# Optimization experiments

Measured on AMD Instinct MI355X. Metric: run time of the kernel, lower is better.

## Reference

```python
import jax, jax.numpy as jnp
import numpy as np

B, T, HID = 4, 4096, 768
H, D = 12, 64
N_HASHES = 2
BUCKET_SIZE = T // 32          # reformer repo config: max_seq_len // 32 = 128
N_BUCKETS = T // BUCKET_SIZE   # 32
SELF_ATTN_VALUE = -5e4         # reformer_pytorch TOKEN_SELF_ATTN_VALUE
MASK_VALUE = -1e9


def lsh_attention(X, mask_bool, W_qk, W_v, rotations):
    # X: [b, t, hid]; rotations: [d, n_hashes, n_buckets//2] (shared across batch & heads)
    b, t, _ = X.shape
    d, n_hashes, half_nb = rotations.shape
    n_buckets = 2 * half_nb
    h = W_qk.shape[0] // d
    scale = d ** -0.5

    qk = X @ W_qk.T            # shared query/key projection (bias-free in reformer_pytorch)
    v = X @ W_v.T

    def merge_heads(x):  # [b,t,h*d] -> [b*h, t, d]
        return x.reshape(b, t, h, d).transpose(0, 2, 1, 3).reshape(b * h, t, d)

    qk, v = merge_heads(qk), merge_heads(v)
    maskbh = jnp.repeat(mask_bool, h, axis=0)          # [bh, t]

    # --- LSH bucketing ---
    rotated = jnp.einsum('btf,fhi->bhti', qk, rotations)          # [bh, nh, t, nb/2]
    rotated = jnp.concatenate([rotated, -rotated], axis=-1)       # [bh, nh, t, nb]
    buckets = jnp.argmax(rotated, axis=-1)                        # [bh, nh, t]
    offsets = (jnp.arange(n_hashes) * n_buckets)[None, :, None]
    buckets = (buckets + offsets).reshape(b * h, n_hashes * t)

    # --- stable sort by (bucket, position) ---
    total = n_hashes * t
    ticker = jnp.arange(total)[None, :]
    buckets_and_t = buckets * t + (ticker % t)
    sticker = jnp.argsort(buckets_and_t, axis=-1)   # stable
    undo = jnp.argsort(sticker, axis=-1)
    st = sticker % t                                 # original positions, sorted order

    sqk = jnp.take_along_axis(qk, st[..., None], axis=1)
    sv = jnp.take_along_axis(v, st[..., None], axis=1)
    smask = jnp.take_along_axis(maskbh, st, axis=1)

    # --- chunk; each chunk attends to itself + previous chunk ---
    n_chunks = n_hashes * n_buckets
    cl = total // n_chunks                                  # == bucket_size
    bq_t = st.reshape(b * h, n_chunks, cl)
    bqk = sqk.reshape(b * h, n_chunks, cl, d)
    bv = sv.reshape(b * h, n_chunks, cl, d)
    bmask = smask.reshape(b * h, n_chunks, cl)

    bq = bqk
    bk = bqk / jnp.clip(jnp.linalg.norm(bqk, axis=-1, keepdims=True), 1e-12)

    def look_one_back(x):
        return jnp.concatenate([x, jnp.roll(x, 1, axis=1)], axis=2)

    bk, bv = look_one_back(bk), look_one_back(bv)
    bkv_t = look_one_back(bq_t)
    bkv_mask = look_one_back(bmask)

    dots = jnp.einsum('bnie,bnje->bnij', bq, bk) * scale    # [bh, n_chunks, cl, 2cl]
    pad = bmask[..., :, None] & bkv_mask[..., None, :]
    dots = jnp.where(pad, dots, MASK_VALUE)
    self_mask = bq_t[..., :, None] == bkv_t[..., None, :]
    dots = jnp.where(self_mask, SELF_ATTN_VALUE, dots)

    lse = jax.scipy.special.logsumexp(dots, axis=-1, keepdims=True)
    probs = jnp.exp(dots - lse)
    bo = jnp.einsum('bnij,bnje->bnie', probs, bv)

    # --- unsort and combine hash rounds via softmax over round logsumexps ---
    so = bo.reshape(b * h, total, d)
    slogits = lse.reshape(b * h, total)
    o = jnp.take_along_axis(so, undo[..., None], axis=1)
    logits = jnp.take_along_axis(slogits, undo, axis=1)

    o = o.reshape(b * h, n_hashes, t, d)
    logits = logits.reshape(b * h, n_hashes, t, 1)
    round_probs = jnp.exp(logits - jax.scipy.special.logsumexp(logits, axis=1, keepdims=True))
    out = jnp.sum(o * round_probs, axis=1)                  # [bh, t, d]
    return out.reshape(b, h, t, d).transpose(0, 2, 1, 3).reshape(b, t, h * d)


def setup_inputs() -> dict:
    key = jax.random.key(0)
    ks = jax.random.split(key, 8)
    s = 1.0 / np.sqrt(HID)
    return {
        'X': jax.random.normal(ks[0], (B, T, HID), jnp.float32),
        'mask': jnp.ones((B, T), jnp.float32),
        'W_qk': jax.random.uniform(ks[1], (H * D, HID), jnp.float32, -s, s),
        'W_v': jax.random.uniform(ks[2], (H * D, HID), jnp.float32, -s, s),
        'rotations': jax.random.normal(ks[3], (D, N_HASHES, N_BUCKETS // 2), jnp.float32),
        'W_to': jax.random.uniform(ks[4], (HID, H * D), jnp.float32, -s, s),
        'b_to': jnp.zeros((HID,), jnp.float32),
        'W_o': jax.random.uniform(ks[5], (HID, HID), jnp.float32, -s, s),
        'b_o': jnp.zeros((HID,), jnp.float32),
    }


def reference(X, mask, W_qk, W_v, rotations, W_to, b_to, W_o, b_o):
    attn = lsh_attention(X, mask.astype(bool), W_qk, W_v, rotations)
    attn = attn @ W_to.T + b_to     # LSHSelfAttention.to_out
    return attn @ W_o.T + b_o       # ReformerAttention.W_o
```

## Files before the change

kernel.cpp:

```cpp
#include <hip/hip_runtime.h>
#include <hip/hip_bf16.h>
#include <math.h>


typedef __attribute__((ext_vector_type(8))) short bf16x8;
typedef __attribute__((ext_vector_type(4))) float f32x4;
typedef __attribute__((ext_vector_type(4))) double f64x4;

__device__ __forceinline__ float bf_lo(unsigned int w) { return __uint_as_float(w << 16); }
__device__ __forceinline__ float bf_hi(unsigned int w) { return __uint_as_float(w & 0xffff0000u); }
__device__ __forceinline__ float load_in(const void* p, size_t i, bool f32) {
  return f32 ? ((const float*)p)[i]
             : __bfloat162float(((const __hip_bfloat16*)p)[i]);
}
__device__ __forceinline__ unsigned short f2bf(float x) {
  __hip_bfloat16 h = __float2bfloat16(x);
  return *reinterpret_cast<unsigned short*>(&h);
}
__device__ __forceinline__ float bf2f(unsigned short u) { return __uint_as_float(((unsigned int)u) << 16); }

__global__ void k_detect(const unsigned int* __restrict__ X, int* __restrict__ flag) {
  if (threadIdx.x == 0 && blockIdx.x == 0) {
    int vote = 0;
    for (int i = 0; i < 64; ++i) {
      unsigned int e = (X[i] >> 7) & 0xffu;
      vote += (e >= 100u && e <= 141u) ? 1 : 0;
    }
    *flag = (vote < 32) ? 1 : 0;
  }
}

__global__ __launch_bounds__(256) void k_convert(
    const void* __restrict__ src, unsigned short* __restrict__ dst, int n8,
    const int* __restrict__ flag) {
  const bool f32in = (*flag != 0);
  int i = blockIdx.x * 256 + threadIdx.x;
  if (i >= n8) return;
  if (f32in) {
    const float4* s = (const float4*)src + (size_t)i * 2;
    float4 a = s[0], b = s[1];
    union { unsigned short u[8]; uint4 v; } o;
    o.u[0] = f2bf(a.x); o.u[1] = f2bf(a.y); o.u[2] = f2bf(a.z); o.u[3] = f2bf(a.w);
    o.u[4] = f2bf(b.x); o.u[5] = f2bf(b.y); o.u[6] = f2bf(b.z); o.u[7] = f2bf(b.w);
    ((uint4*)dst)[i] = o.v;
  } else {
    ((uint4*)dst)[i] = ((const uint4*)src)[i];
  }
}

__global__ __launch_bounds__(256) void k_build_wrot(
    const void* __restrict__ Wqk, const void* __restrict__ rot,
    double* __restrict__ WrotT, const int* __restrict__ flag) {
  const bool f32in = (*flag != 0);
  int idx = blockIdx.x * 256 + threadIdx.x;
  if (idx >= 768 * 384) return;
  int row = idx % 384;
  int c   = idx / 384;
  int hh = row >> 5, hi = row & 31;
  double s = 0.0;
  for (int f = 0; f < 64; ++f) {
    double rv = (double)load_in(rot, f * 32 + hi, f32in);
    double wv = (double)load_in(Wqk, (size_t)(hh * 64 + f) * 768 + c, f32in);
    s = fma(rv, wv, s);
  }
  WrotT[(size_t)c * 384 + row] = s;
}

__global__ __launch_bounds__(512) void k_bucket(
    const void* __restrict__ X, const double* __restrict__ WrotT,
    unsigned char* __restrict__ cls, const int* __restrict__ flag) {
  const bool f32in = (*flag != 0);
  __shared__ double SH[7296];
  double* Sc = SH;
  const int tid = threadIdx.x;
  const int M0 = blockIdx.x * 128;
  const int N0 = blockIdx.y * 96;
  const int w = tid >> 6, lane = tid & 63;
  const int l15 = lane & 15, lq = lane >> 4;
  const int sr = tid >> 2, sh2 = tid & 3;
  const int wk = tid >> 5, wn3 = (tid & 31) * 3;

  f64x4 acc[6];
  #pragma unroll
  for (int j = 0; j < 6; ++j) acc[j] = (f64x4){0.0, 0.0, 0.0, 0.0};

  int rowid[4], colid[4];
  {
    f64x4 zz = (f64x4){0.0, 0.0, 0.0, 0.0};
    f64x4 pr = __builtin_amdgcn_mfma_f64_16x16x4f64(
        (double)l15, (lq == 0) ? 1.0 : 0.0, zz, 0, 0, 0);
    f64x4 pc = __builtin_amdgcn_mfma_f64_16x16x4f64(
        (lq == 0) ? 1.0 : 0.0, (double)l15, zz, 0, 0, 0);
    #pragma unroll
    for (int r = 0; r < 4; ++r) {
      rowid[r] = (int)pr[r];
      colid[r] = (int)pc[r];
    }
  }

  double xv[4];
  double wvv[3];
  auto load_chunk = [&](int k0) {
    size_t base = (size_t)(M0 + sr) * 768 + k0 + sh2 * 4;
    if (f32in) {
      float4 f0 = *(const float4*)((const float*)X + base);
      xv[0] = f0.x; xv[1] = f0.y; xv[2] = f0.z; xv[3] = f0.w;
    } else {
      uint2 u = *(const uint2*)((const unsigned short*)X + base);
      xv[0] = (double)bf_lo(u.x); xv[1] = (double)bf_hi(u.x);
      xv[2] = (double)bf_lo(u.y); xv[3] = (double)bf_hi(u.y);
    }
    const double* wp = WrotT + (size_t)(k0 + wk) * 384 + N0 + wn3;
    wvv[0] = wp[0]; wvv[1] = wp[1]; wvv[2] = wp[2];
  };
  auto store_stage = [&](int bsel) {
    double* Xs = SH + bsel * 2080;
    double* Ws = SH + 4160 + bsel * 1568;
    #pragma unroll
    for (int j = 0; j < 4; ++j) Xs[(sh2 * 4 + j) * 130 + sr] = xv[j];
    Ws[wk * 98 + wn3]     = wvv[0];
    Ws[wk * 98 + wn3 + 1] = wvv[1];
    Ws[wk * 98 + wn3 + 2] = wvv[2];
  };

  load_chunk(0);
  store_stage(0);
  __syncthreads();
  for (int t = 0; t < 48; ++t) {
    const double* Xs = SH + (t & 1) * 2080;
    const double* Ws = SH + 4160 + (t & 1) * 1568;
    if (t < 47) load_chunk((t + 1) * 16);
    #pragma unroll
    for (int kq = 0; kq < 4; ++kq) {
      double a = Xs[(kq * 4 + lq) * 130 + w * 16 + l15];
      const double* wr = &Ws[(kq * 4 + lq) * 98 + l15];
      #pragma unroll
      for (int nt = 0; nt < 6; ++nt)
        acc[nt] = __builtin_amdgcn_mfma_f64_16x16x4f64(a, wr[nt * 16], acc[nt], 0, 0, 0);
    }
    if (t < 47) store_stage((t & 1) ^ 1);
    __syncthreads();
  }

  #pragma unroll
  for (int chunk = 0; chunk < 2; ++chunk) {
    __syncthreads();
    if ((w >> 2) == chunk) {
      int lr = (w & 3) * 16;
      #pragma unroll
      for (int nt = 0; nt < 6; ++nt)
        #pragma unroll
        for (int r = 0; r < 4; ++r)
          Sc[(nt * 16 + colid[r]) * 66 + lr + rowid[r]] = acc[nt][r];
    }
    __syncthreads();
    for (int task = tid; task < 384; task += 512) {
      int g = task >> 6, tok = task & 63;
      const double* s = &Sc[(g * 16) * 66 + tok];
      double mx = -1.0e300;
      #pragma unroll
      for (int i = 0; i < 16; ++i) {
        double a = s[i * 66];
        mx = fmax(mx, fmax(a, -a));
      }
      int amax = 0;
      #pragma unroll
      for (int i = 15; i >= 0; --i) if (-s[i * 66] == mx) amax = 16 + i;
      #pragma unroll
      for (int i = 15; i >= 0; --i) if (s[i * 66] == mx) amax = i;
      int m = M0 + chunk * 64 + tok;
      int b = m >> 12, t = m & 4095;
      int gg = blockIdx.y * 6 + g, hh = gg >> 1, h = gg & 1;
      cls[(size_t)(b * 12 + hh) * 8192 + h * 4096 + t] = (unsigned char)(h * 32 + amax);
    }
  }
}

__global__ __launch_bounds__(1024) void k_sort(
    const unsigned char* __restrict__ clsg,
    unsigned short* __restrict__ stick) {
  __shared__ unsigned short cntg[128 * 64];
  __shared__ int classbase[64];
  const int row = blockIdx.x;
  const int tid = threadIdx.x;
  const int wave = tid >> 6, lane = tid & 63;
  const unsigned char* cr = clsg + ((size_t)row << 13);

  for (int i = tid; i < 128 * 64 / 2; i += 1024) ((uint32_t*)cntg)[i] = 0;
  __syncthreads();

  unsigned char myc[8], myrank[8];
  const unsigned long long ltmask = (lane == 0) ? 0ull : (~0ull >> (64 - lane));
  #pragma unroll
  for (int chunk = 0; chunk < 8; ++chunk) {
    int g = chunk * 16 + wave;
    int j = g * 64 + lane;
    int c = cr[j];
    unsigned long long same = ~0ull;
    #pragma unroll
    for (int bit = 0; bit < 6; ++bit) {
      unsigned long long bm = __ballot((c >> bit) & 1);
      same &= ((c >> bit) & 1) ? bm : ~bm;
    }
    int rank = __popcll(same & ltmask);
    if (rank == 0) cntg[g * 64 + c] = (unsigned short)__popcll(same);
    myc[chunk] = (unsigned char)c;
    myrank[chunk] = (unsigned char)rank;
  }
  __syncthreads();
  if (tid < 64) {
    int run = 0;
    for (int g = 0; g < 128; ++g) {
      int t = cntg[g * 64 + tid];
      cntg[g * 64 + tid] = (unsigned short)run;
      run += t;
    }
    classbase[tid] = run;
  }
  __syncthreads();
  if (tid == 0) {
    int run = 0;
    for (int c = 0; c < 64; ++c) { int t = classbase[c]; classbase[c] = run; run += t; }
  }
  __syncthreads();
  unsigned short* out = stick + ((size_t)row << 13);
  #pragma unroll
  for (int chunk = 0; chunk < 8; ++chunk) {
    int g = chunk * 16 + wave;
    int j = g * 64 + lane;
    int c = myc[chunk];
    int pos = classbase[c] + cntg[g * 64 + c] + myrank[chunk];
    out[pos] = (unsigned short)j;
  }
}

__global__ __launch_bounds__(256) void k_gemm_mfma(
    const unsigned short* __restrict__ A, const unsigned short* __restrict__ W,
    const void* __restrict__ bias, void* __restrict__ Cout,
    int layout, int out_ext, const int* __restrict__ flag) {
  const bool f32in = (*flag != 0);
  const bool oF32 = out_ext && f32in;
  __shared__ unsigned short As[128 * 40];
  __shared__ unsigned short Bs[128 * 40];
  const int tid = threadIdx.x;
  const int bm = blockIdx.x, bn = blockIdx.y;
  const int w = tid >> 6, lane = tid & 63;
  const int l15 = lane & 15, lq = lane >> 4;
  const int wm = (w >> 1) * 64, wn = (w & 1) * 64;
  const int r4 = tid >> 2, c4 = tid & 3;
  const unsigned short* Ag = A + (size_t)(bm * 128 + r4) * 768 + c4 * 8;
  const unsigned short* Bg = W + (size_t)(bn * 128 + r4) * 768 + c4 * 8;
  f32x4 acc[4][4];
  #pragma unroll
  for (int i = 0; i < 4; ++i)
    #pragma unroll
    for (int j = 0; j < 4; ++j) acc[i][j] = (f32x4){0.f, 0.f, 0.f, 0.f};
  uint4 pa0 = *(const uint4*)(Ag);
  uint4 pa1 = *(const uint4*)(Ag + 64 * 768);
  uint4 pb0 = *(const uint4*)(Bg);
  uint4 pb1 = *(const uint4*)(Bg + 64 * 768);
  for (int kt = 0; kt < 24; ++kt) {
    __syncthreads();
    *(uint4*)&As[r4 * 40 + c4 * 8] = pa0;
    *(uint4*)&As[(r4 + 64) * 40 + c4 * 8] = pa1;
    *(uint4*)&Bs[r4 * 40 + c4 * 8] = pb0;
    *(uint4*)&Bs[(r4 + 64) * 40 + c4 * 8] = pb1;
    __syncthreads();
    if (kt < 23) {
      int off = (kt + 1) * 32;
      pa0 = *(const uint4*)(Ag + off);
      pa1 = *(const uint4*)(Ag + 64 * 768 + off);
      pb0 = *(const uint4*)(Bg + off);
      pb1 = *(const uint4*)(Bg + 64 * 768 + off);
    }
    bf16x8 af[4], bfr[4];
    #pragma unroll
    for (int mt = 0; mt < 4; ++mt)
      af[mt] = *(const bf16x8*)&As[(wm + mt * 16 + l15) * 40 + lq * 8];
    #pragma unroll
    for (int nt = 0; nt < 4; ++nt)
      bfr[nt] = *(const bf16x8*)&Bs[(wn + nt * 16 + l15) * 40 + lq * 8];
    #pragma unroll
    for (int mt = 0; mt < 4; ++mt)
      #pragma unroll
      for (int nt = 0; nt < 4; ++nt)
        acc[mt][nt] = __builtin_amdgcn_mfma_f32_16x16x32_bf16(af[mt], bfr[nt], acc[mt][nt], 0, 0, 0);
  }
  #pragma unroll
  for (int mt = 0; mt < 4; ++mt) {
    #pragma unroll
    for (int nt = 0; nt < 4; ++nt) {
      #pragma unroll
      for (int reg = 0; reg < 4; ++reg) {
        int m = bm * 128 + wm + mt * 16 + lq * 4 + reg;
        int n = bn * 128 + wn + nt * 16 + l15;
        float val = acc[mt][nt][reg];
        if (bias != nullptr) val += load_in(bias, n, f32in);
        if (layout == 0) {
          size_t addr = (size_t)m * 768 + n;
          if (oF32) ((float*)Cout)[addr] = val;
          else      ((unsigned short*)Cout)[addr] = f2bf(val);
        } else {
          int b2 = m >> 12, t2 = m & 4095, hh = n >> 6, f = n & 63;
          ((unsigned short*)Cout)[((((size_t)(b2 * 12 + hh)) << 12) + t2) * 64 + f] = f2bf(val);
        }
      }
    }
  }
}

__global__ __launch_bounds__(256) void k_norm(
    const unsigned short* __restrict__ qk, float* __restrict__ nk) {
  int row = blockIdx.x * 32 + (threadIdx.x >> 3);
  int cs = threadIdx.x & 7;
  const uint4* p = (const uint4*)(qk + (size_t)row * 64);
  uint4 wv = p[cs];
  float s = 0.f;
  float e;
  e = bf_lo(wv.x); s += e * e;  e = bf_hi(wv.x); s += e * e;
  e = bf_lo(wv.y); s += e * e;  e = bf_hi(wv.y); s += e * e;
  e = bf_lo(wv.z); s += e * e;  e = bf_hi(wv.z); s += e * e;
  e = bf_lo(wv.w); s += e * e;  e = bf_hi(wv.w); s += e * e;
  s += __shfl_xor(s, 1, 64);
  s += __shfl_xor(s, 2, 64);
  s += __shfl_xor(s, 4, 64);
  if (cs == 0) nk[row] = 1.0f / fmaxf(sqrtf(s), 1e-12f);
}

__global__ __launch_bounds__(256) void k_attn_mfma(
    const unsigned short* __restrict__ qk,
    const unsigned short* __restrict__ vv,
    const unsigned short* __restrict__ stick,
    const void* __restrict__ mask,
    const float* __restrict__ nk,
    unsigned short* __restrict__ o_r,
    float* __restrict__ lse_r,
    const int* __restrict__ flag) {
  const bool f32in = (*flag != 0);
  __shared__ unsigned short Qs[128 * 72];
  __shared__ unsigned short Ks[64 * 72];
  __shared__ unsigned short Vt[64 * 72];
  __shared__ unsigned short Ps[4 * 32 * 72];
  __shared__ unsigned short Tq[128];
  __shared__ unsigned short Tkv[64];
  __shared__ float Nkv[64];
  unsigned short* Vs = Ps;

  const int tid = threadIdx.x;
  const int bh = blockIdx.x >> 6;
  const int ci = blockIdx.x & 63;
  const int b  = bh / 12;
  const int prev = (ci + 63) & 63;
  const int w = tid >> 6, lane = tid & 63;
  const int l15 = lane & 15, lq = lane >> 4;
  const unsigned short* srow = stick + ((size_t)bh << 13);
  const int jrow = tid >> 3, cs = tid & 7;

  uint4 kreg[2], vreg[2];
  unsigned short tkv_reg[2];
  float nkv_reg[2];
  auto load_kv = [&](int kt) {
    #pragma unroll
    for (int pass = 0; pass < 2; ++pass) {
      int j = jrow + pass * 32;
      int chunk = (kt < 2) ? ci : prev;
      int s = srow[chunk * 128 + (kt & 1) * 64 + j];
      int t = s & 4095;
      kreg[pass] = ((const uint4*)(qk + ((((size_t)bh << 12) + t) << 6)))[cs];
      vreg[pass] = ((const uint4*)(vv + ((((size_t)bh << 12) + t) << 6)))[cs];
      if (cs == 0) {
        float mv = load_in(mask, b * 4096 + t, f32in);
        tkv_reg[pass] = (unsigned short)(t | ((mv != 0.0f) ? 0 : 0x8000));
        nkv_reg[pass] = nk[((size_t)bh << 12) + t] * 0.125f;
      }
    }
  };
  auto store_kv = [&]() {
    #pragma unroll
    for (int pass = 0; pass < 2; ++pass) {
      int j = jrow + pass * 32;
      *(uint4*)&Ks[j * 72 + cs * 8] = kreg[pass];
      int sw = (cs ^ (j & 7) ^ (j >> 3)) & 7;
      *(uint4*)&Vs[j * 72 + sw * 8] = vreg[pass];
      if (cs == 0) { Tkv[j] = tkv_reg[pass]; Nkv[j] = nkv_reg[pass]; }
    }
  };

  load_kv(0);

  #pragma unroll
  for (int pass = 0; pass < 4; ++pass) {
    int r = jrow + pass * 32;
    int s = srow[ci * 128 + r];
    int t = s & 4095;
    uint4 qw = ((const uint4*)(qk + ((((size_t)bh << 12) + t) << 6)))[cs];
    *(uint4*)&Qs[r * 72 + cs * 8] = qw;
    if (cs == 0) {
      float mv = load_in(mask, b * 4096 + t, f32in);
      Tq[r] = (unsigned short)(s | ((mv != 0.0f) ? 0 : 0x8000));
    }
  }
  __syncthreads();

  unsigned short tqr[2][4];
  #pragma unroll
  for (int mt = 0; mt < 2; ++mt)
    #pragma unroll
    for (int reg = 0; reg < 4; ++reg)
      tqr[mt][reg] = Tq[w * 32 + mt * 16 + lq * 4 + reg];

  float m_run[2][4], l_run[2][4];
  f32x4 oacc[2][4];
  #pragma unroll
  for (int mt = 0; mt < 2; ++mt)
    #pragma unroll
    for (int reg = 0; reg < 4; ++reg) { m_run[mt][reg] = -3.0e38f; l_run[mt][reg] = 0.0f; }
  #pragma unroll
  for (int mt = 0; mt < 2; ++mt)
    #pragma unroll
    for (int nto = 0; nto < 4; ++nto) oacc[mt][nto] = (f32x4){0.f, 0.f, 0.f, 0.f};

  for (int kt = 0; kt < 4; ++kt) {
    __syncthreads();
    store_kv();
    if (kt < 3) load_kv(kt + 1);
    __syncthreads();

    #pragma unroll
    for (int i = 0; i < 8; ++i) {
      int cp = w * 8 + i;
      int q8 = cp >> 2;
      int sw = (q8 ^ (lane & 7) ^ (lane >> 3)) & 7;
      uint32_t wv = *(const uint32_t*)&Vs[lane * 72 + sw * 8 + ((2 * cp) & 7)];
      Vt[(2 * cp) * 72 + lane]     = (unsigned short)(wv & 0xffff);
      Vt[(2 * cp + 1) * 72 + lane] = (unsigned short)(wv >> 16);
    }

    f32x4 sacc[2][4];
    #pragma unroll
    for (int mt = 0; mt < 2; ++mt)
      #pragma unroll
      for (int nt = 0; nt < 4; ++nt) sacc[mt][nt] = (f32x4){0.f, 0.f, 0.f, 0.f};
    #pragma unroll
    for (int ks = 0; ks < 2; ++ks) {
      bf16x8 af[2];
      #pragma unroll
      for (int mt = 0; mt < 2; ++mt)
        af[mt] = *(const bf16x8*)&Qs[(w * 32 + mt * 16 + l15) * 72 + ks * 32 + lq * 8];
      #pragma unroll
      for (int nt = 0; nt < 4; ++nt) {
        bf16x8 bfr = *(const bf16x8*)&Ks[(nt * 16 + l15) * 72 + ks * 32 + lq * 8];
        #pragma unroll
        for (int mt = 0; mt < 2; ++mt)
          sacc[mt][nt] = __builtin_amdgcn_mfma_f32_16x16x32_bf16(af[mt], bfr, sacc[mt][nt], 0, 0, 0);
      }
    }

    unsigned short tkc[4];
    float nkc[4];
    #pragma unroll
    for (int nt = 0; nt < 4; ++nt) {
      tkc[nt] = Tkv[nt * 16 + l15];
      nkc[nt] = Nkv[nt * 16 + l15];
    }
    float dv[2][4][4];
    #pragma unroll
    for (int mt = 0; mt < 2; ++mt)
      #pragma unroll
      for (int nt = 0; nt < 4; ++nt)
        #pragma unroll
        for (int reg = 0; reg < 4; ++reg) {
          float x = sacc[mt][nt][reg] * nkc[nt];
          unsigned short ts = tqr[mt][reg];
          if (((tkc[nt] | ts) & 0x8000) != 0) x = -1.0e9f;
          if (((tkc[nt] ^ ts) & 0x0fff) == 0) x = -5.0e4f;
          dv[mt][nt][reg] = x;
        }
    float mn[2][4], scv[2][4];
    #pragma unroll
    for (int mt = 0; mt < 2; ++mt)
      #pragma unroll
      for (int reg = 0; reg < 4; ++reg) {
        float rm = fmaxf(fmaxf(dv[mt][0][reg], dv[mt][1][reg]),
                         fmaxf(dv[mt][2][reg], dv[mt][3][reg]));
        rm = fmaxf(rm, __shfl_xor(rm, 1, 64));
        rm = fmaxf(rm, __shfl_xor(rm, 2, 64));
        rm = fmaxf(rm, __shfl_xor(rm, 4, 64));
        rm = fmaxf(rm, __shfl_xor(rm, 8, 64));
        float mnew = fmaxf(m_run[mt][reg], rm);
        scv[mt][reg] = __expf(m_run[mt][reg] - mnew);
        m_run[mt][reg] = mnew;
        mn[mt][reg] = mnew;
      }
    #pragma unroll
    for (int mt = 0; mt < 2; ++mt)
      #pragma unroll
      for (int nt = 0; nt < 4; ++nt)
        #pragma unroll
        for (int reg = 0; reg < 4; ++reg)
          dv[mt][nt][reg] = __expf(dv[mt][nt][reg] - mn[mt][reg]);
    #pragma unroll
    for (int mt = 0; mt < 2; ++mt)
      #pragma unroll
      for (int reg = 0; reg < 4; ++reg) {
        float rs = ((dv[mt][0][reg] + dv[mt][1][reg]) + (dv[mt][2][reg] + dv[mt][3][reg]));
        rs += __shfl_xor(rs, 1, 64);
        rs += __shfl_xor(rs, 2, 64);
        rs += __shfl_xor(rs, 4, 64);
        rs += __shfl_xor(rs, 8, 64);
        l_run[mt][reg] = l_run[mt][reg] * scv[mt][reg] + rs;
      }
    #pragma unroll
    for (int mt = 0; mt < 2; ++mt)
      #pragma unroll
      for (int nto = 0; nto < 4; ++nto)
        #pragma unroll
        for (int reg = 0; reg < 4; ++reg)
          oacc[mt][nto][reg] *= scv[mt][reg];

    __syncthreads();

    #pragma unroll
    for (int mt = 0; mt < 2; ++mt)
      #pragma unroll
      for (int nt = 0; nt < 4; ++nt)
        #pragma unroll
        for (int reg = 0; reg < 4; ++reg)
          Ps[w * 2304 + (mt * 16 + lq * 4 + reg) * 72 + nt * 16 + l15] = f2bf(dv[mt][nt][reg]);

    #pragma unroll
    for (int ks = 0; ks < 2; ++ks) {
      bf16x8 pf[2];
      #pragma unroll
      for (int mt = 0; mt < 2; ++mt)
        pf[mt] = *(const bf16x8*)&Ps[w * 2304 + (mt * 16 + l15) * 72 + ks * 32 + lq * 8];
      #pragma unroll
      for (int nto = 0; nto < 4; ++nto) {
        bf16x8 vf = *(const bf16x8*)&Vt[(nto * 16 + l15) * 72 + ks * 32 + lq * 8];
        #pragma unroll
        for (int mt = 0; mt < 2; ++mt)
          oacc[mt][nto] = __builtin_amdgcn_mfma_f32_16x16x32_bf16(pf[mt], vf, oacc[mt][nto], 0, 0, 0);
      }
    }
  }

  float invl[2][4];
  #pragma unroll
  for (int mt = 0; mt < 2; ++mt)
    #pragma unroll
    for (int reg = 0; reg < 4; ++reg) {
      float lr = l_run[mt][reg];
      invl[mt][reg] = 1.0f / lr;
      if (l15 == 0) {
        int Rr = w * 32 + mt * 16 + lq * 4 + reg;
        int s = Tq[Rr];
        int tq0 = s & 4095, rq0 = (s >> 12) & 1;
        lse_r[(((size_t)(bh * 2 + rq0)) << 12) + tq0] = m_run[mt][reg] + __logf(lr);
      }
    }
  #pragma unroll
  for (int mt = 0; mt < 2; ++mt)
    #pragma unroll
    for (int nto = 0; nto < 4; ++nto)
      #pragma unroll
      for (int reg = 0; reg < 4; ++reg)
        Ps[w * 2304 + (mt * 16 + lq * 4 + reg) * 72 + nto * 16 + l15] =
            f2bf(oacc[mt][nto][reg] * invl[mt][reg]);
  #pragma unroll
  for (int pass = 0; pass < 4; ++pass) {
    int rl = pass * 8 + (lane >> 3);
    int s = Tq[w * 32 + rl];
    int tq0 = s & 4095, rq0 = (s >> 12) & 1;
    uint4 ov = *(const uint4*)&Ps[w * 2304 + rl * 72 + (lane & 7) * 8];
    *(uint4*)(o_r + ((((size_t)(bh * 2 + rq0)) << 12) + tq0) * 64 + (lane & 7) * 8) = ov;
  }
}

__global__ __launch_bounds__(256) void k_combine(
    const unsigned short* __restrict__ o_r,
    const float* __restrict__ lse_r,
    unsigned short* __restrict__ attn) {
  int idx = blockIdx.x * 256 + threadIdx.x;
  if (idx >= 48 * 4096 * 8) return;
  int f8 = idx & 7;
  int t = (idx >> 3) & 4095;
  int bh = idx >> 15;
  float l0 = lse_r[((size_t)(bh * 2 + 0) << 12) + t];
  float l1 = lse_r[((size_t)(bh * 2 + 1) << 12) + t];
  float mm = fmaxf(l0, l1);
  float e0 = __expf(l0 - mm), e1 = __expf(l1 - mm);
  float inv = 1.0f / (e0 + e1);
  float c0 = e0 * inv, c1 = e1 * inv;
  uint4 v0 = *(const uint4*)(o_r + ((((size_t)(bh * 2 + 0)) << 12) + t) * 64 + f8 * 8);
  uint4 v1 = *(const uint4*)(o_r + ((((size_t)(bh * 2 + 1)) << 12) + t) * 64 + f8 * 8);
  union { unsigned short u[8]; uint4 v; } o;
  const unsigned int* a0 = (const unsigned int*)&v0;
  const unsigned int* a1 = (const unsigned int*)&v1;
  #pragma unroll
  for (int j = 0; j < 4; ++j) {
    float lo = c0 * bf_lo(a0[j]) + c1 * bf_lo(a1[j]);
    float hi = c0 * bf_hi(a0[j]) + c1 * bf_hi(a1[j]);
    o.u[2 * j]     = f2bf(lo);
    o.u[2 * j + 1] = f2bf(hi);
  }
  int b = bh / 12, hh = bh % 12;
  *(uint4*)(attn + ((size_t)(b * 4096 + t)) * 768 + hh * 64 + f8 * 8) = o.v;
}

extern "C" void kernel_launch(void* const* d_in, const int* in_sizes, int n_in,
                              void* d_out, int out_size, void* d_ws, size_t ws_size,
                              hipStream_t stream) {
  (void)in_sizes; (void)n_in; (void)out_size; (void)ws_size;
  const void* X    = d_in[0];
  const void* mask = d_in[1];
  const void* Wqk  = d_in[2];
  const void* Wv   = d_in[3];
  const void* rot  = d_in[4];
  const void* Wto  = d_in[5];
  const void* bto  = d_in[6];
  const void* Wo   = d_in[7];
  const void* bo   = d_in[8];

  char* ws = (char*)d_ws;
  int*            flag  = (int*)(ws);
  unsigned short* stick = (unsigned short*)(ws + 256);
  float*          lse_r = (float*)(ws + 786688);
  float*          nk    = (float*)(ws + 2359552);
  unsigned short* qk    = (unsigned short*)(ws + 3145984);
  unsigned short* v     = (unsigned short*)(ws + 28311808);
  unsigned short* o_r   = (unsigned short*)(ws + 53477632);
  double*         WrotT = (double*)(ws + 53477632);
  unsigned char*  cls   = (unsigned char*)(ws + 55836928);
  unsigned short* Wqkb  = (unsigned short*)(ws + 56230144);
  unsigned short* Wvb   = (unsigned short*)(ws + 57409792);
  unsigned short* Xb    = (unsigned short*)(ws + 58589440);
  unsigned short* Wtob  = (unsigned short*)(ws + 53477632);
  unsigned short* Wob   = (unsigned short*)(ws + 54657280);
  unsigned short* attn  = v;
  unsigned short* tmp   = qk;

  k_detect<<<1, 64, 0, stream>>>((const unsigned int*)X, flag);
  k_convert<<<6144, 256, 0, stream>>>(X, Xb, 1572864, flag);
  k_convert<<<288, 256, 0, stream>>>(Wqk, Wqkb, 73728, flag);
  k_convert<<<288, 256, 0, stream>>>(Wv, Wvb, 73728, flag);
  k_build_wrot<<<1152, 256, 0, stream>>>(Wqk, rot, WrotT, flag);
  k_bucket<<<dim3(128, 4), 512, 0, stream>>>(X, WrotT, cls, flag);
  k_sort<<<48, 1024, 0, stream>>>(cls, stick);
  k_gemm_mfma<<<dim3(128, 6), 256, 0, stream>>>(Xb, Wqkb, nullptr, qk, 1, 0, flag);
  k_gemm_mfma<<<dim3(128, 6), 256, 0, stream>>>(Xb, Wvb,  nullptr, v,  1, 0, flag);
  k_norm<<<6144, 256, 0, stream>>>(qk, nk);
  k_attn_mfma<<<3072, 256, 0, stream>>>(qk, v, stick, mask, nk, o_r, lse_r, flag);
  k_combine<<<6144, 256, 0, stream>>>(o_r, lse_r, attn);
  k_convert<<<288, 256, 0, stream>>>(Wto, Wtob, 73728, flag);
  k_convert<<<288, 256, 0, stream>>>(Wo, Wob, 73728, flag);
  k_gemm_mfma<<<dim3(128, 6), 256, 0, stream>>>(attn, Wtob, bto, tmp, 0, 0, flag);
  k_gemm_mfma<<<dim3(128, 6), 256, 0, stream>>>(tmp, Wob, bo, d_out, 0, 1, flag);
}
```

Before: 650.7 us.

## Alias Q, P and V staging in one LDS buffer and hold Q fragments in registers

Q fragments are loaded into registers once after staging, so the Q shared buffer can be reused for the P tile and the V staging area. That removes a separate 18KB buffer and lowers LDS use per block, allowing more resident blocks. The register prefetch of the next K/V tile is dropped, and K/V are now loaded straight from global memory into LDS after the barrier. This gives up load/compute overlap in exchange for fewer registers and less LDS. The aliasing depends on Q no longer being read from LDS after the fragment load, and on P and V uses not overlapping.

```diff
diff --git a/kernel.cpp b/kernel.cpp
--- a/kernel.cpp
+++ b/kernel.cpp
@@ -337,14 +337,15 @@
     float* __restrict__ lse_r,
     const int* __restrict__ flag) {
   const bool f32in = (*flag != 0);
-  __shared__ unsigned short Qs[128 * 72];
+  __shared__ unsigned short QPs[128 * 72];
   __shared__ unsigned short Ks[64 * 72];
   __shared__ unsigned short Vt[64 * 72];
-  __shared__ unsigned short Ps[4 * 32 * 72];
   __shared__ unsigned short Tq[128];
   __shared__ unsigned short Tkv[64];
   __shared__ float Nkv[64];
-  unsigned short* Vs = Ps;
+  unsigned short* Qs = QPs;
+  unsigned short* Ps = QPs;
+  unsigned short* Vs = QPs;
 
   const int tid = threadIdx.x;
   const int bh = blockIdx.x >> 6;
@@ -356,38 +357,6 @@
   const unsigned short* srow = stick + ((size_t)bh << 13);
   const int jrow = tid >> 3, cs = tid & 7;
 
-  uint4 kreg[2], vreg[2];
-  unsigned short tkv_reg[2];
-  float nkv_reg[2];
-  auto load_kv = [&](int kt) {
-    #pragma unroll
-    for (int pass = 0; pass < 2; ++pass) {
-      int j = jrow + pass * 32;
-      int chunk = (kt < 2) ? ci : prev;
-      int s = srow[chunk * 128 + (kt & 1) * 64 + j];
-      int t = s & 4095;
-      kreg[pass] = ((const uint4*)(qk + ((((size_t)bh << 12) + t) << 6)))[cs];
-      vreg[pass] = ((const uint4*)(vv + ((((size_t)bh << 12) + t) << 6)))[cs];
-      if (cs == 0) {
-        float mv = load_in(mask, b * 4096 + t, f32in);
-        tkv_reg[pass] = (unsigned short)(t | ((mv != 0.0f) ? 0 : 0x8000));
-        nkv_reg[pass] = nk[((size_t)bh << 12) + t] * 0.125f;
-      }
-    }
-  };
-  auto store_kv = [&]() {
-    #pragma unroll
-    for (int pass = 0; pass < 2; ++pass) {
-      int j = jrow + pass * 32;
-      *(uint4*)&Ks[j * 72 + cs * 8] = kreg[pass];
-      int sw = (cs ^ (j & 7) ^ (j >> 3)) & 7;
-      *(uint4*)&Vs[j * 72 + sw * 8] = vreg[pass];
-      if (cs == 0) { Tkv[j] = tkv_reg[pass]; Nkv[j] = nkv_reg[pass]; }
-    }
-  };
-
-  load_kv(0);
-
   #pragma unroll
   for (int pass = 0; pass < 4; ++pass) {
     int r = jrow + pass * 32;
@@ -402,6 +371,13 @@
   }
   __syncthreads();
 
+  bf16x8 qf[2][2];
+  #pragma unroll
+  for (int ks = 0; ks < 2; ++ks)
+    #pragma unroll
+    for (int mt = 0; mt < 2; ++mt)
+      qf[ks][mt] = *(const bf16x8*)&Qs[(w * 32 + mt * 16 + l15) * 72 + ks * 32 + lq * 8];
+
   unsigned short tqr[2][4];
   #pragma unroll
   for (int mt = 0; mt < 2; ++mt)
@@ -422,8 +398,23 @@
 
   for (int kt = 0; kt < 4; ++kt) {
     __syncthreads();
-    store_kv();
-    if (kt < 3) load_kv(kt + 1);
+    #pragma unroll
+    for (int pass = 0; pass < 2; ++pass) {
+      int j = jrow + pass * 32;
+      int chunk = (kt < 2) ? ci : prev;
+      int s = srow[chunk * 128 + (kt & 1) * 64 + j];
+      int t = s & 4095;
+      const uint4* kb = (const uint4*)(qk + ((((size_t)bh << 12) + t) << 6));
+      *(uint4*)&Ks[j * 72 + cs * 8] = kb[cs];
+      const uint4* vb = (const uint4*)(vv + ((((size_t)bh << 12) + t) << 6));
+      int sw = (cs ^ (j & 7) ^ (j >> 3)) & 7;
+      *(uint4*)&Vs[j * 72 + sw * 8] = vb[cs];
+      if (cs == 0) {
+        float mv = load_in(mask, b * 4096 + t, f32in);
+        Tkv[j] = (unsigned short)(t | ((mv != 0.0f) ? 0 : 0x8000));
+        Nkv[j] = nk[((size_t)bh << 12) + t] * 0.125f;
+      }
+    }
     __syncthreads();
 
     #pragma unroll
@@ -443,16 +434,12 @@
       for (int nt = 0; nt < 4; ++nt) sacc[mt][nt] = (f32x4){0.f, 0.f, 0.f, 0.f};
     #pragma unroll
     for (int ks = 0; ks < 2; ++ks) {
-      bf16x8 af[2];
-      #pragma unroll
-      for (int mt = 0; mt < 2; ++mt)
-        af[mt] = *(const bf16x8*)&Qs[(w * 32 + mt * 16 + l15) * 72 + ks * 32 + lq * 8];
       #pragma unroll
       for (int nt = 0; nt < 4; ++nt) {
         bf16x8 bfr = *(const bf16x8*)&Ks[(nt * 16 + l15) * 72 + ks * 32 + lq * 8];
         #pragma unroll
         for (int mt = 0; mt < 2; ++mt)
-          sacc[mt][nt] = __builtin_amdgcn_mfma_f32_16x16x32_bf16(af[mt], bfr, sacc[mt][nt], 0, 0, 0);
+          sacc[mt][nt] = __builtin_amdgcn_mfma_f32_16x16x32_bf16(qf[ks][mt], bfr, sacc[mt][nt], 0, 0, 0);
       }
     }
 
```

New measurement: 620.3 us. 4.7% less time.
